# Kernel optimization log

Measured on AMD Instinct MI355X. Metric: run time of the kernel, lower is better.

## Reference

```python
import jax, jax.numpy as jnp
import numpy as np

N_EMBD = 768
N_HEAD = 12
HEAD_DIM = N_EMBD // N_HEAD


def setup_inputs() -> dict:
    key = jax.random.key(0)
    ks = jax.random.split(key, 5)
    B, S = 4, 2048
    x = jax.random.normal(ks[0], (B, S, N_EMBD), dtype=jnp.float32)
    scale = 0.02
    w_attn = jax.random.normal(ks[1], (N_EMBD, 3 * N_EMBD), dtype=jnp.float32) * scale
    b_attn = jnp.zeros((3 * N_EMBD,), dtype=jnp.float32)
    w_proj = jax.random.normal(ks[2], (N_EMBD, N_EMBD), dtype=jnp.float32) * scale
    b_proj = jnp.zeros((N_EMBD,), dtype=jnp.float32)
    return {"x": x, "w_attn": w_attn, "b_attn": b_attn, "w_proj": w_proj, "b_proj": b_proj}


def reference(x, w_attn, b_attn, w_proj, b_proj):
    B, S, E = x.shape
    qkv = x @ w_attn + b_attn  # [B,S,3E]
    q, k, v = jnp.split(qkv, 3, axis=2)
    # [B,H,S,D]
    q = q.reshape(B, S, N_HEAD, HEAD_DIM).transpose(0, 2, 1, 3)
    k = k.reshape(B, S, N_HEAD, HEAD_DIM).transpose(0, 2, 1, 3)
    v = v.reshape(B, S, N_HEAD, HEAD_DIM).transpose(0, 2, 1, 3)
    scores = jnp.einsum('bhqd,bhkd->bhqk', q, k) / jnp.sqrt(jnp.float32(HEAD_DIM))
    causal = jnp.tril(jnp.ones((S, S), dtype=bool))
    scores = jnp.where(causal[None, None], scores, jnp.float32(-jnp.inf))
    weights = jax.nn.softmax(scores, axis=-1)
    out = jnp.einsum('bhqk,bhkd->bhqd', weights, v)
    out = out.transpose(0, 2, 1, 3).reshape(B, S, E)
    return out @ w_proj + b_proj
```

## Files before the change

### kernel.cpp

```cpp
#include <hip/hip_runtime.h>
#include <hip/hip_bf16.h>

typedef __attribute__((ext_vector_type(8))) __bf16 bf16x8;
typedef __attribute__((ext_vector_type(4))) __bf16 bf16x4;
typedef __attribute__((ext_vector_type(4))) float f32x4;

#define E_ 768
#define HEADS 12
#define HD 64
#define S_ 2048
#define B_ 4

__device__ inline unsigned short f2bf(float f) {
    union { float f; unsigned int u; } x{f};
    unsigned int r = x.u + 0x7FFFu + ((x.u >> 16) & 1u);
    return (unsigned short)(r >> 16);
}

__device__ inline float fexp2(float x) { return __builtin_amdgcn_exp2f(x); }

__global__ void cvt_kernel(const float* __restrict__ in, unsigned short* __restrict__ out, int n4) {
    int i = blockIdx.x * blockDim.x + threadIdx.x;
    if (i < n4) {
        float4 v = reinterpret_cast<const float4*>(in)[i];
        ushort4 o;
        o.x = f2bf(v.x); o.y = f2bf(v.y); o.z = f2bf(v.z); o.w = f2bf(v.w);
        reinterpret_cast<ushort4*>(out)[i] = o;
    }
}

__global__ void transpose_cvt(const float* __restrict__ w, unsigned short* __restrict__ wT,
                              int K, int N) {
    __shared__ float tile[32][33];
    int n0 = blockIdx.x * 32, k0 = blockIdx.y * 32;
    int tx = threadIdx.x, ty = threadIdx.y;
    tile[ty][tx] = w[(size_t)(k0 + ty) * N + n0 + tx];
    __syncthreads();
    wT[(size_t)(n0 + ty) * K + k0 + tx] = f2bf(tile[tx][ty]);
}

template<int MODE>
__global__ __launch_bounds__(256) void gemm16(
    const unsigned short* __restrict__ A, const unsigned short* __restrict__ Bt,
    const float* __restrict__ bias,
    unsigned short* __restrict__ Qo, unsigned short* __restrict__ Ko,
    unsigned short* __restrict__ Vt, float* __restrict__ Of,
    int M, int N, int K)
{
    constexpr int BN = 64;
    constexpr int NJ = 2;
    __shared__ unsigned short Sh[128 * 64 + 64 * 64];
    unsigned short* Ash = Sh;
    unsigned short* Bsh = Sh + 128 * 64;

    const int nbx = N / BN;
    const int nwg = (M >> 7) * nbx;
    const int cpx = nwg >> 3;
    const int orig = blockIdx.x;
    const int wgid = (orig & 7) * cpx + (orig >> 3);
    const int row0 = (wgid / nbx) * 128;
    const int col0 = (wgid % nbx) * BN;

    const int t = threadIdx.x;
    const int w = t >> 6, lane = t & 63;
    const int lr = lane & 15, lc = lane >> 4;
    const int wrow = (w >> 1) * 64;
    const int wcol = (w & 1) * 32;

    const int srow = lane >> 3;
    const int sslot = lane & 7;

    f32x4 acc[4][NJ] = {};

    for (int k0 = 0; k0 < K; k0 += 64) {
#pragma unroll
        for (int j = 0; j < 4; j++) {
            const int rbase = j * 32 + w * 8;
            const unsigned short* ga = A + (size_t)(row0 + rbase + srow) * K + k0 + sslot * 8;
            __builtin_amdgcn_global_load_lds(
                (const __attribute__((address_space(1))) void*)ga,
                (__attribute__((address_space(3))) void*)&Ash[rbase * 64], 16, 0, 0);
        }
#pragma unroll
        for (int j = 0; j < NJ; j++) {
            const int rbase = j * 32 + w * 8;
            const unsigned short* gb = Bt + (size_t)(col0 + rbase + srow) * K + k0 + sslot * 8;
            __builtin_amdgcn_global_load_lds(
                (const __attribute__((address_space(1))) void*)gb,
                (__attribute__((address_space(3))) void*)&Bsh[rbase * 64], 16, 0, 0);
        }
        __syncthreads();

#pragma unroll
        for (int ks = 0; ks < 2; ks++) {
            bf16x8 a[4], b[NJ];
#pragma unroll
            for (int i = 0; i < 4; i++)
                a[i] = *reinterpret_cast<const bf16x8*>(&Ash[(wrow + i * 16 + lr) * 64 + ks * 32 + lc * 8]);
#pragma unroll
            for (int j2 = 0; j2 < NJ; j2++)
                b[j2] = *reinterpret_cast<const bf16x8*>(&Bsh[(wcol + j2 * 16 + lr) * 64 + ks * 32 + lc * 8]);
#pragma unroll
            for (int i = 0; i < 4; i++)
#pragma unroll
                for (int j2 = 0; j2 < NJ; j2++)
                    acc[i][j2] = __builtin_amdgcn_mfma_f32_16x16x32_bf16(a[i], b[j2], acc[i][j2], 0, 0, 0);
        }
        __syncthreads();
    }

    if constexpr (MODE == 0) {
        const int bb = row0 >> 11;
        const int s0 = row0 & (S_ - 1);
        const int which = col0 / E_;
        const int h = (col0 - which * E_) >> 6;
        const size_t bh = (size_t)(bb * HEADS + h);
        if (which == 2) {
            __syncthreads();
#pragma unroll
            for (int i = 0; i < 4; i++)
#pragma unroll
                for (int j = 0; j < NJ; j++) {
                    const int c = wcol + j * 16 + lr;
                    const float bv = bias[col0 + c];
#pragma unroll
                    for (int r = 0; r < 4; r++) {
                        const int row = wrow + i * 16 + lc * 4 + r;
                        Sh[c * 128 + (row ^ ((c & 15) << 3))] = f2bf(acc[i][j][r] + bv);
                    }
                }
            __syncthreads();
#pragma unroll
            for (int pass = 0; pass < 4; pass++) {
                const int c = pass * 16 + (t >> 4);
                const int sL = (t & 15) * 8;
                bf16x8 vv = *reinterpret_cast<const bf16x8*>(&Sh[c * 128 + (sL ^ ((c & 15) << 3))]);
                *reinterpret_cast<bf16x8*>(&Vt[(bh * HD + c) * S_ + s0 + sL]) = vv;
            }
            return;
        }
        const float qsc = (which == 0) ? 0.18033688f : 1.0f;
        unsigned short* dst = (which == 0) ? Qo : Ko;
        __syncthreads();
#pragma unroll
        for (int i = 0; i < 4; i++)
#pragma unroll
            for (int j = 0; j < NJ; j++) {
                const int c = wcol + j * 16 + lr;
                const float bv = bias[col0 + c];
#pragma unroll
                for (int r = 0; r < 4; r++) {
                    const int row = wrow + i * 16 + lc * 4 + r;
                    Sh[row * 64 + (c ^ ((row & 7) << 3))] = f2bf((acc[i][j][r] + bv) * qsc);
                }
            }
        __syncthreads();
#pragma unroll
        for (int pass = 0; pass < 4; pass++) {
            const int row = pass * 32 + (t >> 3);
            const int c2 = (t & 7) * 8;
            bf16x8 vv = *reinterpret_cast<const bf16x8*>(&Sh[row * 64 + (c2 ^ ((row & 7) << 3))]);
            *reinterpret_cast<bf16x8*>(&dst[(bh * S_ + s0 + row) * HD + c2]) = vv;
        }
    } else {
#pragma unroll
        for (int i = 0; i < 4; i++)
#pragma unroll
            for (int j = 0; j < NJ; j++) {
                int col = col0 + wcol + j * 16 + lr;
                float bv = bias[col];
#pragma unroll
                for (int r = 0; r < 4; r++) {
                    int row = row0 + wrow + i * 16 + lc * 4 + r;
                    Of[(size_t)row * N + col] = acc[i][j][r] + bv;
                }
            }
    }
}

__global__ __launch_bounds__(256) void attn_kernel(
    const unsigned short* __restrict__ Q, const unsigned short* __restrict__ Kd,
    const unsigned short* __restrict__ Vt, unsigned short* __restrict__ O)
{
    __shared__ unsigned short Ksh[128 * 64];
    __shared__ unsigned short Vsh[64 * 128];

    const int t = threadIdx.x;
    const int w = t >> 6, lane = t & 63;
    const int lr = lane & 15, lc = lane >> 4;
    const int g = blockIdx.x;
    const int tile = 31 - g / 48;
    const int bh = g % 48;
    const int qrow0 = tile * 64 + w * 16;
    const int nIter = (tile + 2) >> 1;

    const unsigned short* Qb = Q + (size_t)bh * S_ * HD;
    const unsigned short* Kb = Kd + (size_t)bh * S_ * HD;
    const unsigned short* Vb = Vt + (size_t)bh * HD * S_;

    const int srK = t >> 3, ssK = t & 7;
    const int kws = ((ssK ^ (srK & 7)) << 3);
    const int srV = t >> 4, ssV = t & 15;
    const int vs1 = (ssV >> 2) * 4 + (ssV & 1) * 2;
    const int voff = ((ssV >> 1) & 1) * 4;
    const int vws1 = ((vs1 ^ srV) << 3) + voff;
    const int vws2 = (((vs1 + 1) ^ srV) << 3) + voff;
    const int r7 = lr & 7;

    const unsigned short* KbS = Kb + (size_t)srK * HD + ssK * 8;
    const unsigned short* VbS = Vb + (size_t)srV * S_ + ssV * 8;

    bf16x8 aq0, aq1;
    aq0 = *reinterpret_cast<const bf16x8*>(Qb + (size_t)(qrow0 + lr) * HD + lc * 8);
    aq1 = *reinterpret_cast<const bf16x8*>(Qb + (size_t)(qrow0 + lr) * HD + 32 + lc * 8);

    f32x4 o[4] = {};
    float m = -INFINITY, l = 0.f;
    const int bb = bh / HEADS, hh = bh - bb * HEADS;
    const int qrow = qrow0 + lr;

    bf16x8 kreg[4], vreg[4];
#pragma unroll
    for (int i = 0; i < 4; i++) {
        kreg[i] = *reinterpret_cast<const bf16x8*>(KbS + i * 32 * HD);
        vreg[i] = *reinterpret_cast<const bf16x8*>(VbS + i * 16 * S_);
    }

    for (int it = 0; it < nIter; ++it) {
        __syncthreads();
#pragma unroll
        for (int i = 0; i < 4; i++) {
            *reinterpret_cast<bf16x8*>(&Ksh[(srK + i * 32) * 64 + kws]) = kreg[i];
            union { bf16x8 v; bf16x4 h[2]; } u;
            u.v = vreg[i];
            const int vrow = (srV + i * 16) * 128;
            *reinterpret_cast<bf16x4*>(&Vsh[vrow + vws1]) = u.h[0];
            *reinterpret_cast<bf16x4*>(&Vsh[vrow + vws2]) = u.h[1];
        }
        __syncthreads();

        if (it + 1 < nIter) {
            const int nkv0 = (it + 1) * 128;
#pragma unroll
            for (int i = 0; i < 4; i++) {
                kreg[i] = *reinterpret_cast<const bf16x8*>(KbS + (size_t)nkv0 * HD + i * 32 * HD);
                vreg[i] = *reinterpret_cast<const bf16x8*>(VbS + nkv0 + i * 16 * S_);
            }
        }

        const int kv0 = it * 128;
        const bool needMask = (it == nIter - 1);

        float p[8][4];
#pragma unroll
        for (int kt = 0; kt < 8; kt++) {
            const int row = kt * 16 + lr;
            const bf16x8 bk0 = *reinterpret_cast<const bf16x8*>(&Ksh[row * 64 + ((lc ^ r7) << 3)]);
            const bf16x8 bk1 = *reinterpret_cast<const bf16x8*>(&Ksh[row * 64 + (((4 + lc) ^ r7) << 3)]);
            f32x4 s = {};
            s = __builtin_amdgcn_mfma_f32_16x16x32_bf16(bk0, aq0, s, 0, 0, 0);
            s = __builtin_amdgcn_mfma_f32_16x16x32_bf16(bk1, aq1, s, 0, 0, 0);
#pragma unroll
            for (int r = 0; r < 4; r++) p[kt][r] = s[r];
        }
        if (needMask) {
#pragma unroll
            for (int kt = 0; kt < 8; kt++) {
                const int kbase = kv0 + kt * 16 + lc * 4;
#pragma unroll
                for (int r = 0; r < 4; r++)
                    if (kbase + r > qrow) p[kt][r] = -1e30f;
            }
        }

        float rm = -1e30f;
#pragma unroll
        for (int kt = 0; kt < 8; kt++)
#pragma unroll
            for (int r = 0; r < 4; r++) rm = fmaxf(rm, p[kt][r]);
        rm = fmaxf(rm, __shfl_xor(rm, 16));
        rm = fmaxf(rm, __shfl_xor(rm, 32));

        const bool grow = !__all(rm <= m);
        float mn = m, sc;
        if (grow) {
            mn = fmaxf(m, rm);
            sc = fexp2(m - mn);
        }

        float rs = 0.f;
#pragma unroll
        for (int kt = 0; kt < 8; kt++)
#pragma unroll
            for (int r = 0; r < 4; r++) {
                float e = fexp2(p[kt][r] - mn);
                p[kt][r] = e; rs += e;
            }
        rs += __shfl_xor(rs, 16);
        rs += __shfl_xor(rs, 32);

        if (grow) {
            l = l * sc + rs;
            m = mn;
            float scq[4];
#pragma unroll
            for (int r = 0; r < 4; r++) scq[r] = __shfl(sc, lc * 4 + r);
#pragma unroll
            for (int dt = 0; dt < 4; dt++)
#pragma unroll
                for (int r = 0; r < 4; r++) o[dt][r] *= scq[r];
        } else {
            l += rs;
        }

        bf16x8 ap[4];
#pragma unroll
        for (int kc = 0; kc < 4; kc++) {
            union { bf16x8 v; __bf16 b[8]; } u;
            u.b[0] = (__bf16)p[2 * kc][0];     u.b[1] = (__bf16)p[2 * kc][1];
            u.b[2] = (__bf16)p[2 * kc][2];     u.b[3] = (__bf16)p[2 * kc][3];
            u.b[4] = (__bf16)p[2 * kc + 1][0]; u.b[5] = (__bf16)p[2 * kc + 1][1];
            u.b[6] = (__bf16)p[2 * kc + 1][2]; u.b[7] = (__bf16)p[2 * kc + 1][3];
            ap[kc] = u.v;
        }

#pragma unroll
        for (int dt = 0; dt < 4; dt++) {
            const int row = dt * 16 + lr;
#pragma unroll
            for (int kc = 0; kc < 4; kc++) {
                const bf16x8 bv = *reinterpret_cast<const bf16x8*>(
                    &Vsh[row * 128 + (((kc * 4 + lc) ^ lr) << 3)]);
                o[dt] = __builtin_amdgcn_mfma_f32_16x16x32_bf16(ap[kc], bv, o[dt], 0, 0, 0);
            }
        }
    }

    {
        float lq[4];
#pragma unroll
        for (int r = 0; r < 4; r++) lq[r] = __shfl(l, lc * 4 + r);
#pragma unroll
        for (int r = 0; r < 4; r++) {
            float inv = 1.f / lq[r];
            int qr = qrow0 + lc * 4 + r;
#pragma unroll
            for (int dt = 0; dt < 4; dt++)
                O[((size_t)(bb * S_ + qr)) * E_ + hh * HD + dt * 16 + lr] = f2bf(o[dt][r] * inv);
        }
    }
}

extern "C" void kernel_launch(void* const* d_in, const int* in_sizes, int n_in,
                              void* d_out, int out_size, void* d_ws, size_t ws_size,
                              hipStream_t stream) {
    const float* x      = (const float*)d_in[0];
    const float* w_attn = (const float*)d_in[1];
    const float* b_attn = (const float*)d_in[2];
    const float* w_proj = (const float*)d_in[3];
    const float* b_proj = (const float*)d_in[4];
    float* out = (float*)d_out;

    char* ws = (char*)d_ws;
    const size_t M = (size_t)B_ * S_;
    unsigned short* xb  = (unsigned short*)(ws);
    unsigned short* waT = (unsigned short*)(ws + 12582912);
    unsigned short* wpT = (unsigned short*)(ws + 16121856);
    unsigned short* Qb  = (unsigned short*)(ws + 17301504);
    unsigned short* Kb  = (unsigned short*)(ws + 29884416);
    unsigned short* Vt  = (unsigned short*)(ws + 42467328);
    unsigned short* AO  = (unsigned short*)(ws + 55050240);

    int n4 = (int)(M * E_ / 4);
    cvt_kernel<<<(n4 + 255) / 256, 256, 0, stream>>>(x, xb, n4);
    transpose_cvt<<<dim3(3 * E_ / 32, E_ / 32), dim3(32, 32), 0, stream>>>(w_attn, waT, E_, 3 * E_);
    transpose_cvt<<<dim3(E_ / 32, E_ / 32), dim3(32, 32), 0, stream>>>(w_proj, wpT, E_, E_);

    gemm16<0><<<2304, 256, 0, stream>>>(
        xb, waT, b_attn, Qb, Kb, Vt, nullptr, (int)M, 3 * E_, E_);

    attn_kernel<<<1536, 256, 0, stream>>>(Qb, Kb, Vt, AO);

    gemm16<1><<<768, 256, 0, stream>>>(
        AO, wpT, b_proj, nullptr, nullptr, nullptr, out, (int)M, E_, E_);
}
```

Baseline: 147.3 us.

## Fuse fp32-to-bf16 input conversion into QKV GEMM and interleave attention tile order

Removes the standalone conversion kernel for x. The QKV GEMM now loads fp32 rows into registers, prefetching the next k-slice, and converts them to bf16 while writing LDS, replacing the async global-to-LDS path for A. This avoids an extra pass writing and rereading the bf16 copy of x, at the cost of doubled A read bytes per tile and more register pressure. The attention grid mapping also alternates long and short causal tiles, and redundant epilogue barriers are dropped.

Result: slower. 167.3 us (+13.6%).

```diff
diff --git a/kernel.cpp b/kernel.cpp
--- a/kernel.cpp
+++ b/kernel.cpp
@@ -18,16 +18,6 @@
 }
 
 __device__ inline float fexp2(float x) { return __builtin_amdgcn_exp2f(x); }
-
-__global__ void cvt_kernel(const float* __restrict__ in, unsigned short* __restrict__ out, int n4) {
-    int i = blockIdx.x * blockDim.x + threadIdx.x;
-    if (i < n4) {
-        float4 v = reinterpret_cast<const float4*>(in)[i];
-        ushort4 o;
-        o.x = f2bf(v.x); o.y = f2bf(v.y); o.z = f2bf(v.z); o.w = f2bf(v.w);
-        reinterpret_cast<ushort4*>(out)[i] = o;
-    }
-}
 
 __global__ void transpose_cvt(const float* __restrict__ w, unsigned short* __restrict__ wT,
                               int K, int N) {
@@ -41,6 +31,7 @@
 
 template<int MODE>
 __global__ __launch_bounds__(256) void gemm16(
+    const float* __restrict__ Af,
     const unsigned short* __restrict__ A, const unsigned short* __restrict__ Bt,
     const float* __restrict__ bias,
     unsigned short* __restrict__ Qo, unsigned short* __restrict__ Ko,
@@ -72,14 +63,37 @@
 
     f32x4 acc[4][NJ] = {};
 
+    float4 ar0[4], ar1[4];
+    if constexpr (MODE == 0) {
+#pragma unroll
+        for (int j = 0; j < 4; j++) {
+            const float* gx = Af + (size_t)(row0 + j * 32 + w * 8 + srow) * K + sslot * 8;
+            ar0[j] = *reinterpret_cast<const float4*>(gx);
+            ar1[j] = *reinterpret_cast<const float4*>(gx + 4);
+        }
+    }
+
     for (int k0 = 0; k0 < K; k0 += 64) {
-#pragma unroll
-        for (int j = 0; j < 4; j++) {
-            const int rbase = j * 32 + w * 8;
-            const unsigned short* ga = A + (size_t)(row0 + rbase + srow) * K + k0 + sslot * 8;
-            __builtin_amdgcn_global_load_lds(
-                (const __attribute__((address_space(1))) void*)ga,
-                (__attribute__((address_space(3))) void*)&Ash[rbase * 64], 16, 0, 0);
+        if constexpr (MODE == 0) {
+#pragma unroll
+            for (int j = 0; j < 4; j++) {
+                const int rbase = j * 32 + w * 8;
+                bf16x8 pk;
+                pk[0] = (__bf16)ar0[j].x; pk[1] = (__bf16)ar0[j].y;
+                pk[2] = (__bf16)ar0[j].z; pk[3] = (__bf16)ar0[j].w;
+                pk[4] = (__bf16)ar1[j].x; pk[5] = (__bf16)ar1[j].y;
+                pk[6] = (__bf16)ar1[j].z; pk[7] = (__bf16)ar1[j].w;
+                *reinterpret_cast<bf16x8*>(&Ash[(rbase + srow) * 64 + sslot * 8]) = pk;
+            }
+        } else {
+#pragma unroll
+            for (int j = 0; j < 4; j++) {
+                const int rbase = j * 32 + w * 8;
+                const unsigned short* ga = A + (size_t)(row0 + rbase + srow) * K + k0 + sslot * 8;
+                __builtin_amdgcn_global_load_lds(
+                    (const __attribute__((address_space(1))) void*)ga,
+                    (__attribute__((address_space(3))) void*)&Ash[rbase * 64], 16, 0, 0);
+            }
         }
 #pragma unroll
         for (int j = 0; j < NJ; j++) {
@@ -90,6 +104,17 @@
                 (__attribute__((address_space(3))) void*)&Bsh[rbase * 64], 16, 0, 0);
         }
         __syncthreads();
+
+        if constexpr (MODE == 0) {
+            if (k0 + 64 < K) {
+#pragma unroll
+                for (int j = 0; j < 4; j++) {
+                    const float* gx = Af + (size_t)(row0 + j * 32 + w * 8 + srow) * K + (k0 + 64) + sslot * 8;
+                    ar0[j] = *reinterpret_cast<const float4*>(gx);
+                    ar1[j] = *reinterpret_cast<const float4*>(gx + 4);
+                }
+            }
+        }
 
 #pragma unroll
         for (int ks = 0; ks < 2; ks++) {
@@ -116,7 +141,6 @@
         const int h = (col0 - which * E_) >> 6;
         const size_t bh = (size_t)(bb * HEADS + h);
         if (which == 2) {
-            __syncthreads();
 #pragma unroll
             for (int i = 0; i < 4; i++)
 #pragma unroll
@@ -141,7 +165,6 @@
         }
         const float qsc = (which == 0) ? 0.18033688f : 1.0f;
         unsigned short* dst = (which == 0) ? Qo : Ko;
-        __syncthreads();
 #pragma unroll
         for (int i = 0; i < 4; i++)
 #pragma unroll
@@ -189,7 +212,8 @@
     const int w = t >> 6, lane = t & 63;
     const int lr = lane & 15, lc = lane >> 4;
     const int g = blockIdx.x;
-    const int tile = 31 - g / 48;
+    const int u = g / 48;
+    const int tile = (u & 1) ? (u >> 1) : (31 - (u >> 1));
     const int bh = g % 48;
     const int qrow0 = tile * 64 + w * 16;
     const int nIter = (tile + 2) >> 1;
@@ -231,11 +255,11 @@
 #pragma unroll
         for (int i = 0; i < 4; i++) {
             *reinterpret_cast<bf16x8*>(&Ksh[(srK + i * 32) * 64 + kws]) = kreg[i];
-            union { bf16x8 v; bf16x4 h[2]; } u;
-            u.v = vreg[i];
+            union { bf16x8 v; bf16x4 h[2]; } u2;
+            u2.v = vreg[i];
             const int vrow = (srV + i * 16) * 128;
-            *reinterpret_cast<bf16x4*>(&Vsh[vrow + vws1]) = u.h[0];
-            *reinterpret_cast<bf16x4*>(&Vsh[vrow + vws2]) = u.h[1];
+            *reinterpret_cast<bf16x4*>(&Vsh[vrow + vws1]) = u2.h[0];
+            *reinterpret_cast<bf16x4*>(&Vsh[vrow + vws2]) = u2.h[1];
         }
         __syncthreads();
 
@@ -316,12 +340,12 @@
         bf16x8 ap[4];
 #pragma unroll
         for (int kc = 0; kc < 4; kc++) {
-            union { bf16x8 v; __bf16 b[8]; } u;
-            u.b[0] = (__bf16)p[2 * kc][0];     u.b[1] = (__bf16)p[2 * kc][1];
-            u.b[2] = (__bf16)p[2 * kc][2];     u.b[3] = (__bf16)p[2 * kc][3];
-            u.b[4] = (__bf16)p[2 * kc + 1][0]; u.b[5] = (__bf16)p[2 * kc + 1][1];
-            u.b[6] = (__bf16)p[2 * kc + 1][2]; u.b[7] = (__bf16)p[2 * kc + 1][3];
-            ap[kc] = u.v;
+            union { bf16x8 v; __bf16 b[8]; } u2;
+            u2.b[0] = (__bf16)p[2 * kc][0];     u2.b[1] = (__bf16)p[2 * kc][1];
+            u2.b[2] = (__bf16)p[2 * kc][2];     u2.b[3] = (__bf16)p[2 * kc][3];
+            u2.b[4] = (__bf16)p[2 * kc + 1][0]; u2.b[5] = (__bf16)p[2 * kc + 1][1];
+            u2.b[6] = (__bf16)p[2 * kc + 1][2]; u2.b[7] = (__bf16)p[2 * kc + 1][3];
+            ap[kc] = u2.v;
         }
 
 #pragma unroll
@@ -363,7 +387,6 @@
 
     char* ws = (char*)d_ws;
     const size_t M = (size_t)B_ * S_;
-    unsigned short* xb  = (unsigned short*)(ws);
     unsigned short* waT = (unsigned short*)(ws + 12582912);
     unsigned short* wpT = (unsigned short*)(ws + 16121856);
     unsigned short* Qb  = (unsigned short*)(ws + 17301504);
@@ -371,16 +394,14 @@
     unsigned short* Vt  = (unsigned short*)(ws + 42467328);
     unsigned short* AO  = (unsigned short*)(ws + 55050240);
 
-    int n4 = (int)(M * E_ / 4);
-    cvt_kernel<<<(n4 + 255) / 256, 256, 0, stream>>>(x, xb, n4);
     transpose_cvt<<<dim3(3 * E_ / 32, E_ / 32), dim3(32, 32), 0, stream>>>(w_attn, waT, E_, 3 * E_);
     transpose_cvt<<<dim3(E_ / 32, E_ / 32), dim3(32, 32), 0, stream>>>(w_proj, wpT, E_, E_);
 
     gemm16<0><<<2304, 256, 0, stream>>>(
-        xb, waT, b_attn, Qb, Kb, Vt, nullptr, (int)M, 3 * E_, E_);
+        x, nullptr, waT, b_attn, Qb, Kb, Vt, nullptr, (int)M, 3 * E_, E_);
 
     attn_kernel<<<1536, 256, 0, stream>>>(Qb, Kb, Vt, AO);
 
     gemm16<1><<<768, 256, 0, stream>>>(
-        AO, wpT, b_proj, nullptr, nullptr, nullptr, out, (int)M, E_, E_);
+        nullptr, AO, wpT, b_proj, nullptr, nullptr, nullptr, out, (int)M, E_, E_);
 }
```
